# Kernel optimization log

Hardware: AMD Instinct MI355X
Metric: run time of the kernel (lower is better)

## Reference

```python
import jax, jax.numpy as jnp
import numpy as np

# ---- config (mirrors conf dict passed to RegionLoss.__init__) ----
ANCHORS = jnp.array([[1.3221, 1.73145], [3.19275, 4.00944], [5.05587, 8.09892],
                     [9.47112, 4.84053], [11.2364, 10.0071]], dtype=jnp.float32)
NUM_CLASSES = 80
OBJECT_SCALE = 5.0
NO_OBJECT_SCALE = 1.0
CLASS_SCALE = 1.0
COORD_SCALE = 1.0
SIL_THRESH = 0.6
SEEN = 0  # fresh module -> seen < 12800 warm-start branch is active


def _iou_center(a, b):
    """IoU of center-format boxes (cx, cy, w, h); a, b broadcastable [..., 4]."""
    ax1, ax2 = a[..., 0] - a[..., 2] * 0.5, a[..., 0] + a[..., 2] * 0.5
    ay1, ay2 = a[..., 1] - a[..., 3] * 0.5, a[..., 1] + a[..., 3] * 0.5
    bx1, bx2 = b[..., 0] - b[..., 2] * 0.5, b[..., 0] + b[..., 2] * 0.5
    by1, by2 = b[..., 1] - b[..., 3] * 0.5, b[..., 1] + b[..., 3] * 0.5
    iw = jnp.maximum(jnp.minimum(ax2, bx2) - jnp.maximum(ax1, bx1), 0.0)
    ih = jnp.maximum(jnp.minimum(ay2, by2) - jnp.maximum(ay1, by1), 0.0)
    inter = iw * ih
    union = a[..., 2] * a[..., 3] + b[..., 2] * b[..., 3] - inter
    return inter / union


def setup_inputs() -> dict:
    key = jax.random.key(0)
    k1, k2, k3, k4 = jax.random.split(key, 4)
    B, A, C, H, W, NBOX = 32, 5, NUM_CLASSES, 52, 52, 50
    pred = jax.random.normal(k1, (B, A * (C + 5), H, W), dtype=jnp.float32)
    cls = jax.random.randint(k2, (B, NBOX, 1), 0, C).astype(jnp.float32)
    xy = jax.random.uniform(k3, (B, NBOX, 2), minval=0.02, maxval=0.98, dtype=jnp.float32)
    wh = jax.random.uniform(k4, (B, NBOX, 2), minval=0.05, maxval=0.4, dtype=jnp.float32)
    target = jnp.concatenate([cls, xy, wh], axis=-1)  # (B, NBOX, 5): cls,x,y,w,h in [0,1]
    return {"pred": pred, "target": target, "train_out": 0}


def _region_loss(pred, target):
    B, H, W = pred.shape[0], pred.shape[2], pred.shape[3]
    A, C = ANCHORS.shape[0], NUM_CLASSES
    nbox = target.shape[1]
    p = pred.reshape(B, A, C + 5, H, W)

    txy = jax.nn.sigmoid(p[:, :, 0:2])                 # (B,A,2,H,W)
    twh = p[:, :, 2:4]                                 # (B,A,2,H,W)
    pred_no_off = jnp.concatenate([txy, twh], axis=2)  # (B,A,4,H,W)
    pred_conf = jax.nn.sigmoid(p[:, :, 4])             # (B,A,H,W)
    cls_logits = p[:, :, 5:]                           # (B,A,C,H,W)

    # decode boxes to grid units (detached in the original)
    grid_x = jnp.arange(W, dtype=p.dtype)              # broadcasts along W (last dim)
    grid_y = jnp.arange(H, dtype=p.dtype)[:, None]     # broadcasts along H
    aw = ANCHORS[:, 0][None, :, None, None]
    ah = ANCHORS[:, 1][None, :, None, None]
    bx = txy[:, :, 0] + grid_x
    by = txy[:, :, 1] + grid_y
    bw = jnp.exp(twh[:, :, 0]) * aw
    bh = jnp.exp(twh[:, :, 1]) * ah
    pred_boxes = jax.lax.stop_gradient(jnp.stack([bx, by, bw, bh], axis=-1))  # (B,A,H,W,4)

    # ground truth in grid units
    scale = jnp.array([W, H, W, H], dtype=p.dtype)
    gt = target[:, :, 1:5] * scale                     # (B,nbox,4) center format
    valid = target[:, :, 1] > 0                        # sentinel: x == 0 terminates

    # conf mask: zero-out cells whose best IoU vs any GT exceeds sil_thresh
    pb_flat = pred_boxes.reshape(B, A * H * W, 4)
    ious = _iou_center(gt[:, :, None, :], pb_flat[:, None, :, :])  # (B,nbox,A*H*W)
    ious = jnp.where(valid[:, :, None], ious, 0.0)
    max_iou = jnp.max(ious, axis=1).reshape(B, A, H, W)
    conf_mask = jnp.where(max_iou > SIL_THRESH, 0.0, NO_OBJECT_SCALE)

    # best anchor per GT via width/height-only IoU (boxes at origin)
    gw, gh = gt[..., 2], gt[..., 3]
    inter = jnp.minimum(gw[..., None], ANCHORS[:, 0]) * jnp.minimum(gh[..., None], ANCHORS[:, 1])
    union = gw[..., None] * gh[..., None] + ANCHORS[:, 0] * ANCHORS[:, 1] - inter
    best_a = jnp.argmax(inter / union, axis=-1)        # (B,nbox)

    gi = jnp.clip(gt[..., 0].astype(jnp.int32), 0, W - 1)
    gj = jnp.clip(gt[..., 1].astype(jnp.int32), 0, H - 1)
    b_idx = jnp.broadcast_to(jnp.arange(B)[:, None], (B, nbox))
    bi = jnp.where(valid, b_idx, B)                    # invalid GTs -> OOB batch, dropped

    aw_b = ANCHORS[best_a, 0]
    ah_b = ANCHORS[best_a, 1]
    tx_t = gt[..., 0] - gi.astype(p.dtype)
    ty_t = gt[..., 1] - gj.astype(p.dtype)
    tw_t = jnp.log(gw / aw_b)
    th_t = jnp.log(gh / ah_b)

    pred_box_at = pred_boxes[b_idx, best_a, gj, gi]    # (B,nbox,4) decoded box at GT cell
    iou_gt = _iou_center(gt, pred_box_at)              # (B,nbox)

    # initialize targets/masks (seen < 12800 warm start)
    if SEEN < 12800:
        coord_mask = jnp.ones((B, A, H, W), dtype=p.dtype)
        target_box = jnp.zeros((B, A, 4, H, W), dtype=p.dtype).at[:, :, 0:2].set(0.5)
    else:
        coord_mask = jnp.zeros((B, A, H, W), dtype=p.dtype)
        target_box = jnp.zeros((B, A, 4, H, W), dtype=p.dtype)
    cls_mask = jnp.zeros((B, A, H, W), dtype=p.dtype)
    target_conf = jnp.zeros((B, A, H, W), dtype=p.dtype)
    target_cls = jnp.zeros((B, A, H, W), dtype=p.dtype)

    coord_mask = coord_mask.at[bi, best_a, gj, gi].set(1.0, mode='drop')
    cls_mask = cls_mask.at[bi, best_a, gj, gi].set(1.0, mode='drop')
    conf_mask = conf_mask.at[bi, best_a, gj, gi].set(OBJECT_SCALE, mode='drop')
    target_box = target_box.at[bi, best_a, 0, gj, gi].set(tx_t, mode='drop')
    target_box = target_box.at[bi, best_a, 1, gj, gi].set(ty_t, mode='drop')
    target_box = target_box.at[bi, best_a, 2, gj, gi].set(tw_t, mode='drop')
    target_box = target_box.at[bi, best_a, 3, gj, gi].set(th_t, mode='drop')
    target_conf = target_conf.at[bi, best_a, gj, gi].set(iou_gt, mode='drop')
    target_cls = target_cls.at[bi, best_a, gj, gi].set(target[:, :, 0], mode='drop')

    # losses
    half = jnp.asarray(0.5, p.dtype)
    loss_x = COORD_SCALE * jnp.sum(((pred_no_off[:, :, 0] - target_box[:, :, 0]) * coord_mask) ** 2) * half
    loss_y = COORD_SCALE * jnp.sum(((pred_no_off[:, :, 1] - target_box[:, :, 1]) * coord_mask) ** 2) * half
    loss_w = COORD_SCALE * jnp.sum(((pred_no_off[:, :, 2] - target_box[:, :, 2]) * coord_mask) ** 2) * half
    loss_h = COORD_SCALE * jnp.sum(((pred_no_off[:, :, 3] - target_box[:, :, 3]) * coord_mask) ** 2) * half
    loss_conf = jnp.sum(((pred_conf - target_conf) * jnp.sqrt(conf_mask)) ** 2) * half

    logp = jax.nn.log_softmax(cls_logits, axis=2)      # (B,A,C,H,W)
    tcls = jnp.clip(target_cls.astype(jnp.int32), 0, C - 1)
    ce = -jnp.take_along_axis(logp, tcls[:, :, None], axis=2)[:, :, 0]  # (B,A,H,W)
    loss_cls = CLASS_SCALE * jnp.sum(cls_mask * ce)

    loss = loss_x + loss_y + loss_w + loss_h + loss_conf + loss_cls
    return loss, loss_x, loss_y, loss_w, loss_h, loss_conf, loss_cls


def reference(pred, target, train_out):
    out = _region_loss(pred, target)
    if train_out:
        return out
    return out[0]
```

## Files before the change

kernel.cpp:

```cpp
#include <hip/hip_runtime.h>
#include <math.h>

#define BB 32
#define AA 5
#define CC 80
#define HH 52
#define WW 52
#define NBOX 50
#define HWSZ (HH*WW)
#define CELLS (AA*HWSZ)

__constant__ float d_aw[AA] = {1.3221f, 3.19275f, 5.05587f, 9.47112f, 11.2364f};
__constant__ float d_ah[AA] = {1.73145f, 4.00944f, 8.09892f, 4.84053f, 10.0071f};

__device__ __forceinline__ float sig(float x) { return 1.f / (1.f + expf(-x)); }

__global__ __launch_bounds__(256) void region_fused(const float* __restrict__ pred,
                                                    const float* __restrict__ target,
                                                    float* __restrict__ out) {
    __shared__ float4 s_box[NBOX];
    __shared__ float2 s_ac[NBOX];
    __shared__ float4 s_t[NBOX];
    __shared__ float2 s_m[NBOX];
    __shared__ float wsum[4];

    const int b = blockIdx.y;
    const int tid = threadIdx.x;

    if (tid < NBOX) {
        const float* t = target + ((size_t)b * NBOX + tid) * 5;
        float t0 = t[0], t1 = t[1], t2 = t[2], t3 = t[3], t4 = t[4];
        float gx = t1 * (float)WW, gy = t2 * (float)HH;
        float gw = t3 * (float)WW, gh = t4 * (float)HH;
        bool valid = t1 > 0.f;
        int best = 0; float bestv = -1.f;
        #pragma unroll
        for (int a = 0; a < AA; ++a) {
            float inter = fminf(gw, d_aw[a]) * fminf(gh, d_ah[a]);
            float uni = gw * gh + d_aw[a] * d_ah[a] - inter;
            float r = inter / uni;
            if (r > bestv) { bestv = r; best = a; }
        }
        int gi = (int)gx; gi = gi < 0 ? 0 : (gi > WW - 1 ? WW - 1 : gi);
        int gj = (int)gy; gj = gj < 0 ? 0 : (gj > HH - 1 ? HH - 1 : gj);

        size_t bbase = ((size_t)(b * AA + best) * (CC + 5)) * HWSZ + (size_t)gj * WW + gi;
        float px = sig(pred[bbase]) + (float)gi;
        float py = sig(pred[bbase + HWSZ]) + (float)gj;
        float pw = expf(pred[bbase + 2 * HWSZ]) * d_aw[best];
        float ph = expf(pred[bbase + 3 * HWSZ]) * d_ah[best];

        float ax1 = gx - gw * 0.5f, ax2 = gx + gw * 0.5f;
        float ay1 = gy - gh * 0.5f, ay2 = gy + gh * 0.5f;
        float bx1 = px - pw * 0.5f, bx2 = px + pw * 0.5f;
        float by1 = py - ph * 0.5f, by2 = py + ph * 0.5f;
        float iw = fmaxf(fminf(ax2, bx2) - fmaxf(ax1, bx1), 0.f);
        float ih = fmaxf(fminf(ay2, by2) - fmaxf(ay1, by1), 0.f);
        float inter = iw * ih;
        float iou_gt = inter / (gw * gh + pw * ph - inter);

        if (valid) {
            s_box[tid] = make_float4(ax1, ax2, ay1, ay2);
            s_ac[tid]  = make_float2(gw * gh, (float)(best * HWSZ + gj * WW + gi));
        } else {
            s_box[tid] = make_float4(0.f, 0.f, 0.f, 0.f);
            s_ac[tid]  = make_float2(0.f, -1.f);
        }
        s_t[tid] = make_float4(gx - (float)gi, gy - (float)gj,
                               logf(gw / d_aw[best]), logf(gh / d_ah[best]));
        s_m[tid] = make_float2(iou_gt, t0);
    }
    __syncthreads();

    const int c = blockIdx.x * 256 + tid;
    float lsum = 0.f;
    if (c < CELLS) {
        int a = c / HWSZ;
        int rem = c - a * HWSZ;
        int hh = rem / WW;
        int wwi = rem - hh * WW;
        size_t base = ((size_t)(b * AA + a) * (CC + 5)) * HWSZ + rem;
        float p0 = pred[base];
        float p1 = pred[base + HWSZ];
        float p2 = pred[base + 2 * HWSZ];
        float p3 = pred[base + 3 * HWSZ];
        float p4 = pred[base + 4 * HWSZ];
        float tx = sig(p0);
        float ty = sig(p1);
        float conf = sig(p4);
        float bx = tx + (float)wwi;
        float by = ty + (float)hh;
        float bw = expf(p2) * d_aw[a];
        float bh = expf(p3) * d_ah[a];
        float px1 = bx - bw * 0.5f, px2 = bx + bw * 0.5f;
        float py1 = by - bh * 0.5f, py2 = by + bh * 0.5f;
        float parea = bw * bh;
        float cf = (float)c;

        float maxiou = 0.f;
        int win = -1;
        #pragma unroll 2
        for (int j = 0; j < NBOX; ++j) {
            float4 r0 = s_box[j];
            float2 r1 = s_ac[j];
            float iw2 = fmaxf(fminf(px2, r0.y) - fmaxf(px1, r0.x), 0.f);
            float ih2 = fmaxf(fminf(py2, r0.w) - fmaxf(py1, r0.z), 0.f);
            float inter2 = iw2 * ih2;
            float iou = inter2 / (parea + r1.x - inter2);
            maxiou = fmaxf(maxiou, iou);
            win = (r1.y == cf) ? j : win;
        }

        float dx, dy, dw, dh, lconf;
        if (win >= 0) {
            float4 r2 = s_t[win];
            float2 r3 = s_m[win];
            dx = tx - r2.x; dy = ty - r2.y; dw = p2 - r2.z; dh = p3 - r2.w;
            float d = conf - r3.x;
            lconf = 2.5f * d * d;
            int tcls = (int)r3.y;
            tcls = tcls < 0 ? 0 : (tcls > CC - 1 ? CC - 1 : tcls);
            const float* lg = pred + base + 5 * (size_t)HWSZ;
            float mx = -INFINITY;
            #pragma unroll 8
            for (int cc = 0; cc < CC; ++cc) mx = fmaxf(mx, lg[(size_t)cc * HWSZ]);
            float s = 0.f;
            #pragma unroll 8
            for (int cc = 0; cc < CC; ++cc) s += expf(lg[(size_t)cc * HWSZ] - mx);
            lsum += (mx + logf(s)) - lg[(size_t)tcls * HWSZ];
        } else {
            dx = tx - 0.5f; dy = ty - 0.5f; dw = p2; dh = p3;
            float cm = (maxiou > 0.6f) ? 0.f : 1.f;
            lconf = 0.5f * cm * conf * conf;
        }
        lsum += 0.5f * (dx * dx + dy * dy + dw * dw + dh * dh) + lconf;
    }

    #pragma unroll
    for (int off = 32; off > 0; off >>= 1)
        lsum += __shfl_down(lsum, off, 64);
    int wave = tid >> 6;
    if ((tid & 63) == 0) wsum[wave] = lsum;
    __syncthreads();
    if (tid == 0) {
        atomicAdd(out, wsum[0] + wsum[1] + wsum[2] + wsum[3]);
    }
}

extern "C" void kernel_launch(void* const* d_in, const int* in_sizes, int n_in,
                              void* d_out, int out_size, void* d_ws, size_t ws_size,
                              hipStream_t stream) {
    const float* pred = (const float*)d_in[0];
    const float* target = (const float*)d_in[1];
    float* out = (float*)d_out;

    hipMemsetAsync(out, 0, sizeof(float) * out_size, stream);
    dim3 grid((CELLS + 255) / 256, BB);
    region_fused<<<grid, dim3(256), 0, stream>>>(pred, target, out);
}
```

Measured before the change: 232.2 us.

## Compute class log-softmax cooperatively per wave and drop IoU division

The per-cell serial 80-class log-softmax on responsible cells is replaced by a wave-cooperative loop: each lane with a matched target is found via ballot, and all 64 lanes load and reduce that cell's class logits in parallel using shuffle max/sum. This removes the divergence where a few lanes serially walk 80 strided loads while the rest of the wave idles. Separately, the max-IoU > 0.6 test is rewritten without division as inter - 0.375*parea > 0.375*garea, and the box loop is unrolled 5. The algebraic rewrite can flip results for IoUs right at the threshold, and the ballot loop serialises per matched cell within a wave.

```diff
diff --git a/kernel.cpp b/kernel.cpp
--- a/kernel.cpp
+++ b/kernel.cpp
@@ -15,6 +15,17 @@
 
 __device__ __forceinline__ float sig(float x) { return 1.f / (1.f + expf(-x)); }
 
+__device__ __forceinline__ float wave_max(float v) {
+    #pragma unroll
+    for (int off = 32; off > 0; off >>= 1) v = fmaxf(v, __shfl_xor(v, off, 64));
+    return v;
+}
+__device__ __forceinline__ float wave_sum(float v) {
+    #pragma unroll
+    for (int off = 32; off > 0; off >>= 1) v += __shfl_xor(v, off, 64);
+    return v;
+}
+
 __global__ __launch_bounds__(256) void region_fused(const float* __restrict__ pred,
                                                     const float* __restrict__ target,
                                                     float* __restrict__ out) {
@@ -26,6 +37,7 @@
 
     const int b = blockIdx.y;
     const int tid = threadIdx.x;
+    const int lane = tid & 63;
 
     if (tid < NBOX) {
         const float* t = target + ((size_t)b * NBOX + tid) * 5;
@@ -61,7 +73,8 @@
 
         if (valid) {
             s_box[tid] = make_float4(ax1, ax2, ay1, ay2);
-            s_ac[tid]  = make_float2(gw * gh, (float)(best * HWSZ + gj * WW + gi));
+            s_ac[tid]  = make_float2(0.375f * gw * gh,
+                                     (float)(best * HWSZ + gj * WW + gi));
         } else {
             s_box[tid] = make_float4(0.f, 0.f, 0.f, 0.f);
             s_ac[tid]  = make_float2(0.f, -1.f);
@@ -74,9 +87,11 @@
 
     const int c = blockIdx.x * 256 + tid;
     float lsum = 0.f;
+    int win = -1;
+    int a = 0, rem = 0, tcls = 0;
     if (c < CELLS) {
-        int a = c / HWSZ;
-        int rem = c - a * HWSZ;
+        a = c / HWSZ;
+        rem = c - a * HWSZ;
         int hh = rem / WW;
         int wwi = rem - hh * WW;
         size_t base = ((size_t)(b * AA + a) * (CC + 5)) * HWSZ + rem;
@@ -94,20 +109,18 @@
         float bh = expf(p3) * d_ah[a];
         float px1 = bx - bw * 0.5f, px2 = bx + bw * 0.5f;
         float py1 = by - bh * 0.5f, py2 = by + bh * 0.5f;
-        float parea = bw * bh;
+        float tp = 0.375f * (bw * bh);
         float cf = (float)c;
 
-        float maxiou = 0.f;
-        int win = -1;
-        #pragma unroll 2
+        bool hit = false;
+        #pragma unroll 5
         for (int j = 0; j < NBOX; ++j) {
             float4 r0 = s_box[j];
             float2 r1 = s_ac[j];
             float iw2 = fmaxf(fminf(px2, r0.y) - fmaxf(px1, r0.x), 0.f);
             float ih2 = fmaxf(fminf(py2, r0.w) - fmaxf(py1, r0.z), 0.f);
             float inter2 = iw2 * ih2;
-            float iou = inter2 / (parea + r1.x - inter2);
-            maxiou = fmaxf(maxiou, iou);
+            hit = hit | ((inter2 - tp) > r1.x);
             win = (r1.y == cf) ? j : win;
         }
 
@@ -118,29 +131,39 @@
             dx = tx - r2.x; dy = ty - r2.y; dw = p2 - r2.z; dh = p3 - r2.w;
             float d = conf - r3.x;
             lconf = 2.5f * d * d;
-            int tcls = (int)r3.y;
-            tcls = tcls < 0 ? 0 : (tcls > CC - 1 ? CC - 1 : tcls);
-            const float* lg = pred + base + 5 * (size_t)HWSZ;
-            float mx = -INFINITY;
-            #pragma unroll 8
-            for (int cc = 0; cc < CC; ++cc) mx = fmaxf(mx, lg[(size_t)cc * HWSZ]);
-            float s = 0.f;
-            #pragma unroll 8
-            for (int cc = 0; cc < CC; ++cc) s += expf(lg[(size_t)cc * HWSZ] - mx);
-            lsum += (mx + logf(s)) - lg[(size_t)tcls * HWSZ];
+            int tc = (int)r3.y;
+            tcls = tc < 0 ? 0 : (tc > CC - 1 ? CC - 1 : tc);
         } else {
             dx = tx - 0.5f; dy = ty - 0.5f; dw = p2; dh = p3;
-            float cm = (maxiou > 0.6f) ? 0.f : 1.f;
-            lconf = 0.5f * cm * conf * conf;
+            lconf = hit ? 0.f : 0.5f * conf * conf;
         }
-        lsum += 0.5f * (dx * dx + dy * dy + dw * dw + dh * dh) + lconf;
+        lsum = 0.5f * (dx * dx + dy * dy + dw * dw + dh * dh) + lconf;
+    }
+
+    unsigned long long mask = __ballot(win >= 0);
+    while (mask) {
+        int src = __ffsll(mask) - 1;
+        mask &= mask - 1;
+        int wa   = __shfl(a, src, 64);
+        int wrem = __shfl(rem, src, 64);
+        int wt   = __shfl(tcls, src, 64);
+        size_t cbase = ((size_t)(b * AA + wa) * (CC + 5) + 5) * HWSZ + (size_t)wrem;
+        float v1 = pred[cbase + (size_t)lane * HWSZ];
+        float v2 = (lane < CC - 64) ? pred[cbase + (size_t)(lane + 64) * HWSZ]
+                                    : -INFINITY;
+        float mx = wave_max(fmaxf(v1, v2));
+        float s = expf(v1 - mx) + ((lane < CC - 64) ? expf(v2 - mx) : 0.f);
+        s = wave_sum(s);
+        float vt = ((lane == wt) ? v1 : 0.f) + ((lane + 64 == wt) ? v2 : 0.f);
+        vt = wave_sum(vt);
+        if (lane == src) lsum += (mx + logf(s)) - vt;
     }
 
     #pragma unroll
     for (int off = 32; off > 0; off >>= 1)
         lsum += __shfl_down(lsum, off, 64);
     int wave = tid >> 6;
-    if ((tid & 63) == 0) wsum[wave] = lsum;
+    if (lane == 0) wsum[wave] = lsum;
     __syncthreads();
     if (tid == 0) {
         atomicAdd(out, wsum[0] + wsum[1] + wsum[2] + wsum[3]);
```

Result: faster. 204.7 us (-11.8%).
